# Optimization experiments

Measured on AMD Instinct MI355X. Metric: run time of the kernel, lower is better.

Reference implementation:

```python
import jax, jax.numpy as jnp
import numpy as np

N_NODES = 50000
N_EDGES = 800000
IN_FEATS = 128
H_FEATS = 128
NUM_CLASSES = 64


def _linear_params(key, fan_in, fan_out):
    kw, kb = jax.random.split(key)
    bound = 1.0 / np.sqrt(fan_in)
    W = jax.random.uniform(kw, (fan_out, fan_in), minval=-bound, maxval=bound, dtype=jnp.float32)
    b = jax.random.uniform(kb, (fan_out,), minval=-bound, maxval=bound, dtype=jnp.float32)
    return W, b


def setup_inputs() -> dict:
    key = jax.random.key(0)
    k_feat, k_src, k_dst, k1, k2, k3 = jax.random.split(key, 6)
    in_feat = jax.random.normal(k_feat, (N_NODES, IN_FEATS), dtype=jnp.float32)
    src = jax.random.randint(k_src, (N_EDGES,), 0, N_NODES, dtype=jnp.int32)
    dst = jax.random.randint(k_dst, (N_EDGES,), 0, N_NODES, dtype=jnp.int32)
    W1, b1 = _linear_params(k1, IN_FEATS, H_FEATS)
    W2, b2 = _linear_params(k2, H_FEATS, H_FEATS)
    W3, b3 = _linear_params(k3, H_FEATS, NUM_CLASSES)
    return {"in_feat": in_feat, "W1": W1, "b1": b1, "W2": W2, "b2": b2,
            "W3": W3, "b3": b3, "src": src, "dst": dst}


def reference(in_feat, W1, b1, W2, b2, W3, b3, src, dst):
    N = in_feat.shape[0]

    def gin_layer(x, W, b):
        # DGL GINConv with eps=0: (x + sum of in-neighbor messages) -> Linear
        agg = jax.ops.segment_sum(x[src], dst, num_segments=N)  # [N, d]
        return jax.nn.relu((x + agg) @ W.T + b)

    h = gin_layer(in_feat, W1, b1)
    h = gin_layer(h, W2, b2)
    h = gin_layer(h, W3, b3)
    return h
```

## Files before the change

kernel.cpp:

```cpp
#include <hip/hip_runtime.h>

typedef _Float16 half8 __attribute__((ext_vector_type(8)));
typedef _Float16 half2v __attribute__((ext_vector_type(2)));
typedef float floatx4 __attribute__((ext_vector_type(4)));
typedef unsigned int uintx4 __attribute__((ext_vector_type(4)));

union AB { uint4 u; half8 h; };
union H2 { unsigned int u; _Float16 h[2]; };
union H2P { unsigned int u; half2v h; };

#define CAPLOG 6
#define CAP 64

__global__ __launch_bounds__(256) void histA_init_k(
    const int* __restrict__ dst, int* __restrict__ histG, int E, int nbins,
    const float* __restrict__ W1, const float* __restrict__ W2, const float* __restrict__ W3,
    _Float16* __restrict__ W1h, _Float16* __restrict__ W2h, _Float16* __restrict__ W3h,
    _Float16* __restrict__ z1, _Float16* __restrict__ h1, _Float16* __restrict__ hZ,
    int n4w1, int n4w2, int n4w3, int zoff128, int zoff64) {
    int t = threadIdx.x;
    if (blockIdx.x < 256) {
        __shared__ int h[256];
        h[t] = 0;
        __syncthreads();
        int per = (E + 255) / 256;
        int beg = blockIdx.x * per;
        int end = min(E, beg + per);
        for (int e = beg + t; e < end; e += 256)
            atomicAdd(&h[dst[e] >> 8], 1);
        __syncthreads();
        for (int i = t; i < nbins; i += 256)
            histG[i * 256 + blockIdx.x] = h[i];
        return;
    }
    int i = (blockIdx.x - 256) * 256 + t;
    const float* X;
    _Float16* O;
    int j;
    if (i < n4w1) { X = W1; O = W1h; j = i; }
    else if (i < n4w1 + n4w2) { X = W2; O = W2h; j = i - n4w1; }
    else if (i < n4w1 + n4w2 + n4w3) { X = W3; O = W3h; j = i - n4w1 - n4w2; }
    else {
        int z = i - (n4w1 + n4w2 + n4w3);
        if (z < 16) ((uint4*)z1)[zoff128 + z] = make_uint4(0, 0, 0, 0);
        else if (z < 32) ((uint4*)h1)[zoff128 + (z - 16)] = make_uint4(0, 0, 0, 0);
        else if (z < 40) ((uint4*)hZ)[zoff64 + (z - 32)] = make_uint4(0, 0, 0, 0);
        return;
    }
    float4 v = reinterpret_cast<const float4*>(X)[j];
    union { uint2 u; _Float16 h[4]; } o;
    o.h[0] = (_Float16)v.x; o.h[1] = (_Float16)v.y;
    o.h[2] = (_Float16)v.z; o.h[3] = (_Float16)v.w;
    reinterpret_cast<uint2*>(O)[j] = o.u;
}

__global__ __launch_bounds__(1024) void scan1_k(const int* __restrict__ x,
                                                int* __restrict__ inc,
                                                int* __restrict__ partial, int n) {
    __shared__ int sd[1024];
    int t = threadIdx.x;
    int v = blockIdx.x * 1024 + t;
    sd[t] = (v < n) ? x[v] : 0;
    __syncthreads();
    for (int off = 1; off < 1024; off <<= 1) {
        int val = (t >= off) ? sd[t - off] : 0;
        __syncthreads();
        sd[t] += val;
        __syncthreads();
    }
    if (v < n) inc[v] = sd[t];
    if (t == 1023) partial[blockIdx.x] = sd[1023];
}

__global__ __launch_bounds__(256) void scatgemm_k(
    const int* __restrict__ src, const int* __restrict__ dst,
    const int* __restrict__ inc, const int* __restrict__ histG,
    const int* __restrict__ partial, int nparts,
    unsigned int* __restrict__ binned, int E, int nbins,
    const float* __restrict__ X, const _Float16* __restrict__ Wh,
    _Float16* __restrict__ z1, int nnodes) {
    constexpr int WSTR = 136;
    __shared__ _Float16 Wl[128 * WSTR];

    const int t = threadIdx.x;
    if (blockIdx.x < 256) {
        int* cur = (int*)Wl;
        int* pp = cur + 256;
        int blk = blockIdx.x;
        if (t < 64) {
            int v = (t < nparts) ? partial[t] : 0;
            for (int off = 1; off < 64; off <<= 1) {
                int n = __shfl_up(v, off, 64);
                if (t >= off) v += n;
            }
            int ex = __shfl_up(v, 1, 64);
            if (t == 0) ex = 0;
            pp[t] = ex;
        }
        __syncthreads();
        for (int i = t; i < nbins; i += 256) {
            int idx = i * 256 + blk;
            cur[i] = inc[idx] + pp[idx >> 10] - histG[idx];
        }
        __syncthreads();
        int per = (E + 255) / 256;
        int beg = blk * per;
        int end = min(E, beg + per);
        for (int e = beg + t; e < end; e += 256) {
            int d = dst[e];
            int s = src[e];
            int pos = atomicAdd(&cur[d >> 8], 1);
            binned[pos] = ((unsigned int)(d & 255) << 16) | (unsigned int)s;
        }
        return;
    }

    for (int p = t; p < 128 * 16; p += 256) {
        int f = p >> 4;
        int kq = (p & 15) * 8;
        *reinterpret_cast<uint4*>(&Wl[f * WSTR + kq]) =
            *reinterpret_cast<const uint4*>(Wh + f * 128 + kq);
    }
    __syncthreads();

    const int wave = t >> 6;
    const int lane = t & 63;
    const int quad = lane >> 4;
    const int fcol = lane & 15;
    const int m_base = ((blockIdx.x - 256) * 4 + wave) * 16;
    const int row = m_base + fcol;
    const bool rowok = row < nnodes;

    floatx4 acc[8];
#pragma unroll
    for (int ft = 0; ft < 8; ft++) acc[ft] = (floatx4){0.f, 0.f, 0.f, 0.f};

    const float* Xrow = X + (size_t)row * 128;
#pragma unroll
    for (int step = 0; step < 4; step++) {
        AB a;
        if (rowok) {
            float4 f0 = *reinterpret_cast<const float4*>(Xrow + step * 32 + quad * 8);
            float4 f1 = *reinterpret_cast<const float4*>(Xrow + step * 32 + quad * 8 + 4);
            a.h[0] = (_Float16)f0.x; a.h[1] = (_Float16)f0.y;
            a.h[2] = (_Float16)f0.z; a.h[3] = (_Float16)f0.w;
            a.h[4] = (_Float16)f1.x; a.h[5] = (_Float16)f1.y;
            a.h[6] = (_Float16)f1.z; a.h[7] = (_Float16)f1.w;
        } else a.u = make_uint4(0u, 0u, 0u, 0u);
#pragma unroll
        for (int ft = 0; ft < 8; ft++) {
            half8 b = *reinterpret_cast<const half8*>(
                &Wl[(ft * 16 + fcol) * WSTR + step * 32 + quad * 8]);
            acc[ft] = __builtin_amdgcn_mfma_f32_16x16x32_f16(a.h, b, acc[ft], 0, 0, 0);
        }
    }

#pragma unroll
    for (int ft = 0; ft < 8; ft++) {
        int f = ft * 16 + fcol;
#pragma unroll
        for (int r = 0; r < 4; r++) {
            int node = m_base + quad * 4 + r;
            if (node < nnodes)
                z1[(size_t)node * 128 + f] = (_Float16)acc[ft][r];
        }
    }
}

__global__ __launch_bounds__(256) void binB_k(const unsigned int* __restrict__ binned,
                                              const int* __restrict__ inc,
                                              const int* __restrict__ histG,
                                              const int* __restrict__ partial, int nparts,
                                              unsigned short* __restrict__ col,
                                              int* __restrict__ cnt,
                                              int N, int E, int nbins) {
    __shared__ unsigned short lcol[256 * CAP];
    __shared__ int lcnt[256];
    __shared__ int pp[64];
    __shared__ int bounds[2];
    int t = threadIdx.x;
    int b = blockIdx.x;
    if (t < 64) {
        int v = (t < nparts) ? partial[t] : 0;
        for (int off = 1; off < 64; off <<= 1) {
            int n = __shfl_up(v, off, 64);
            if (t >= off) v += n;
        }
        int ex = __shfl_up(v, 1, 64);
        if (t == 0) ex = 0;
        pp[t] = ex;
    }
    unsigned int* lcol32 = (unsigned int*)lcol;
    for (int i = t; i < 256 * CAP / 2; i += 256) lcol32[i] = 0xFFFFFFFFu;
    lcnt[t] = 0;
    __syncthreads();
    if (t == 0) {
        int i0 = b * 256;
        bounds[0] = inc[i0] + pp[i0 >> 10] - histG[i0];
    } else if (t == 1) {
        if (b == nbins - 1) bounds[1] = E;
        else {
            int i1 = (b + 1) * 256;
            bounds[1] = inc[i1] + pp[i1 >> 10] - histG[i1];
        }
    }
    __syncthreads();
    int beg = bounds[0], end = bounds[1];
    for (int e = beg + t; e < end; e += 256) {
        unsigned int u = binned[e];
        int dl = u >> 16;
        int pos = atomicAdd(&lcnt[dl], 1);
        if (pos < CAP)
            lcol[(dl << CAPLOG) + ((pos & 3) << 4) + (pos >> 2)] = (unsigned short)(u & 0xFFFFu);
    }
    __syncthreads();
    int base = b << 8;
    int nodes = min(256, N - base);
    uint4* colg = (uint4*)(col + ((size_t)base << CAPLOG));
    const uint4* coll = (const uint4*)lcol;
    for (int i = t; i < nodes * 8; i += 256) colg[i] = coll[i];
    for (int i = t; i < nodes; i += 256) cnt[base + i] = lcnt[i];
}

__global__ __launch_bounds__(256) void agg128_k(const _Float16* __restrict__ Z,
                                                const int* __restrict__ cnt,
                                                const unsigned short* __restrict__ col,
                                                const float* __restrict__ bias,
                                                _Float16* __restrict__ H, int nnodes) {
    int w = blockIdx.x * 4 + (threadIdx.x >> 6);
    int lane = threadIdx.x & 63;
    if (w >= nnodes) return;
    const int q = lane >> 4;
    const int c15 = lane & 15;
    const unsigned int* X32 = reinterpret_cast<const unsigned int*>(Z);
    int deg = cnt[w];
    if (deg > CAP) deg = CAP;
    int nb = (deg + 15) >> 4;
    const unsigned short* c = col + ((size_t)w << CAPLOG) + (q << 4);

    H2P a0[4], a1[4], a2[4], a3[4];
#pragma unroll
    for (int m = 0; m < 4; m++) { a0[m].u = 0u; a1[m].u = 0u; a2[m].u = 0u; a3[m].u = 0u; }

    for (int t = 0; t < nb; t++) {
        uint2 iw = *reinterpret_cast<const uint2*>(c + t * 4);
        int s0 = (int)(iw.x & 0xFFFFu); s0 = (s0 < nnodes) ? s0 : nnodes;
        int s1 = (int)(iw.x >> 16);     s1 = (s1 < nnodes) ? s1 : nnodes;
        int s2 = (int)(iw.y & 0xFFFFu); s2 = (s2 < nnodes) ? s2 : nnodes;
        int s3 = (int)(iw.y >> 16);     s3 = (s3 < nnodes) ? s3 : nnodes;
        uint4 v0 = *reinterpret_cast<const uint4*>(X32 + (size_t)s0 * 64 + c15 * 4);
        uint4 v1 = *reinterpret_cast<const uint4*>(X32 + (size_t)s1 * 64 + c15 * 4);
        uint4 v2 = *reinterpret_cast<const uint4*>(X32 + (size_t)s2 * 64 + c15 * 4);
        uint4 v3 = *reinterpret_cast<const uint4*>(X32 + (size_t)s3 * 64 + c15 * 4);
        H2P u;
        u.u = v0.x; a0[0].h += u.h;  u.u = v0.y; a0[1].h += u.h;
        u.u = v0.z; a0[2].h += u.h;  u.u = v0.w; a0[3].h += u.h;
        u.u = v1.x; a1[0].h += u.h;  u.u = v1.y; a1[1].h += u.h;
        u.u = v1.z; a1[2].h += u.h;  u.u = v1.w; a1[3].h += u.h;
        u.u = v2.x; a2[0].h += u.h;  u.u = v2.y; a2[1].h += u.h;
        u.u = v2.z; a2[2].h += u.h;  u.u = v2.w; a2[3].h += u.h;
        u.u = v3.x; a3[0].h += u.h;  u.u = v3.y; a3[1].h += u.h;
        u.u = v3.z; a3[2].h += u.h;  u.u = v3.w; a3[3].h += u.h;
    }
#pragma unroll
    for (int m = 0; m < 4; m++) {
        a0[m].h += a1[m].h;
        a2[m].h += a3[m].h;
        a0[m].h += a2[m].h;
    }
    float fs[8];
#pragma unroll
    for (int m = 0; m < 4; m++) {
        fs[2 * m] = (float)a0[m].h[0];
        fs[2 * m + 1] = (float)a0[m].h[1];
    }
#pragma unroll
    for (int m = 0; m < 8; m++) fs[m] += __shfl_xor(fs[m], 16, 64);
#pragma unroll
    for (int m = 0; m < 8; m++) fs[m] += __shfl_xor(fs[m], 32, 64);

    if (q == 0) {
        uint4 sv = *reinterpret_cast<const uint4*>(X32 + (size_t)w * 64 + c15 * 4);
        H2 x0, x1, x2, x3;
        x0.u = sv.x; x1.u = sv.y; x2.u = sv.z; x3.u = sv.w;
        float o[8];
        o[0] = (float)x0.h[0] + fs[0]; o[1] = (float)x0.h[1] + fs[1];
        o[2] = (float)x1.h[0] + fs[2]; o[3] = (float)x1.h[1] + fs[3];
        o[4] = (float)x2.h[0] + fs[4]; o[5] = (float)x2.h[1] + fs[5];
        o[6] = (float)x3.h[0] + fs[6]; o[7] = (float)x3.h[1] + fs[7];
        if (bias) {
            float4 b0 = *reinterpret_cast<const float4*>(bias + c15 * 8);
            float4 b1 = *reinterpret_cast<const float4*>(bias + c15 * 8 + 4);
            o[0] = fmaxf(o[0] + b0.x, 0.f); o[1] = fmaxf(o[1] + b0.y, 0.f);
            o[2] = fmaxf(o[2] + b0.z, 0.f); o[3] = fmaxf(o[3] + b0.w, 0.f);
            o[4] = fmaxf(o[4] + b1.x, 0.f); o[5] = fmaxf(o[5] + b1.y, 0.f);
            o[6] = fmaxf(o[6] + b1.z, 0.f); o[7] = fmaxf(o[7] + b1.w, 0.f);
        }
        H2 r0, r1, r2, r3;
        r0.h[0] = (_Float16)o[0]; r0.h[1] = (_Float16)o[1];
        r1.h[0] = (_Float16)o[2]; r1.h[1] = (_Float16)o[3];
        r2.h[0] = (_Float16)o[4]; r2.h[1] = (_Float16)o[5];
        r3.h[0] = (_Float16)o[6]; r3.h[1] = (_Float16)o[7];
        uintx4 ov;
        ov.x = r0.u; ov.y = r1.u; ov.z = r2.u; ov.w = r3.u;
        __builtin_nontemporal_store(
            ov, reinterpret_cast<uintx4*>(reinterpret_cast<unsigned int*>(H) +
                                          (size_t)w * 64 + c15 * 4));
    }
}

__global__ __launch_bounds__(256) void agg_final_k(const _Float16* __restrict__ Z,
                                                   const int* __restrict__ cnt,
                                                   const unsigned short* __restrict__ col,
                                                   const float* __restrict__ bias,
                                                   float* __restrict__ out, int nnodes) {
    int lane = threadIdx.x & 63;
    int sub = lane & 31;
    int node = blockIdx.x * 8 + (threadIdx.x >> 6) * 2 + (lane >> 5);
    if (node >= nnodes) return;
    const int q = sub >> 3;
    const int c7 = sub & 7;
    const unsigned int* Z32 = (const unsigned int*)Z;
    int deg = cnt[node];
    if (deg > CAP) deg = CAP;
    int nb = (deg + 15) >> 4;
    const unsigned short* c = col + ((size_t)node << CAPLOG) + (q << 4);

    H2P a0[4], a1[4], a2[4], a3[4];
#pragma unroll
    for (int m = 0; m < 4; m++) { a0[m].u = 0u; a1[m].u = 0u; a2[m].u = 0u; a3[m].u = 0u; }

    for (int t = 0; t < nb; t++) {
        uint2 iw = *reinterpret_cast<const uint2*>(c + t * 4);
        int s0 = (int)(iw.x & 0xFFFFu); s0 = (s0 < nnodes) ? s0 : nnodes;
        int s1 = (int)(iw.x >> 16);     s1 = (s1 < nnodes) ? s1 : nnodes;
        int s2 = (int)(iw.y & 0xFFFFu); s2 = (s2 < nnodes) ? s2 : nnodes;
        int s3 = (int)(iw.y >> 16);     s3 = (s3 < nnodes) ? s3 : nnodes;
        uint4 v0 = *reinterpret_cast<const uint4*>(Z32 + (size_t)s0 * 32 + c7 * 4);
        uint4 v1 = *reinterpret_cast<const uint4*>(Z32 + (size_t)s1 * 32 + c7 * 4);
        uint4 v2 = *reinterpret_cast<const uint4*>(Z32 + (size_t)s2 * 32 + c7 * 4);
        uint4 v3 = *reinterpret_cast<const uint4*>(Z32 + (size_t)s3 * 32 + c7 * 4);
        H2P u;
        u.u = v0.x; a0[0].h += u.h;  u.u = v0.y; a0[1].h += u.h;
        u.u = v0.z; a0[2].h += u.h;  u.u = v0.w; a0[3].h += u.h;
        u.u = v1.x; a1[0].h += u.h;  u.u = v1.y; a1[1].h += u.h;
        u.u = v1.z; a1[2].h += u.h;  u.u = v1.w; a1[3].h += u.h;
        u.u = v2.x; a2[0].h += u.h;  u.u = v2.y; a2[1].h += u.h;
        u.u = v2.z; a2[2].h += u.h;  u.u = v2.w; a2[3].h += u.h;
        u.u = v3.x; a3[0].h += u.h;  u.u = v3.y; a3[1].h += u.h;
        u.u = v3.z; a3[2].h += u.h;  u.u = v3.w; a3[3].h += u.h;
    }
#pragma unroll
    for (int m = 0; m < 4; m++) {
        a0[m].h += a1[m].h;
        a2[m].h += a3[m].h;
        a0[m].h += a2[m].h;
    }
    float fs[8];
#pragma unroll
    for (int m = 0; m < 4; m++) {
        fs[2 * m] = (float)a0[m].h[0];
        fs[2 * m + 1] = (float)a0[m].h[1];
    }
#pragma unroll
    for (int m = 0; m < 8; m++) fs[m] += __shfl_xor(fs[m], 8, 64);
#pragma unroll
    for (int m = 0; m < 8; m++) fs[m] += __shfl_xor(fs[m], 16, 64);

    if (q == 0) {
        uint4 sv = *reinterpret_cast<const uint4*>(Z32 + (size_t)node * 32 + c7 * 4);
        H2 x0, x1, x2, x3;
        x0.u = sv.x; x1.u = sv.y; x2.u = sv.z; x3.u = sv.w;
        float4 b0 = *reinterpret_cast<const float4*>(bias + c7 * 8);
        float4 b1 = *reinterpret_cast<const float4*>(bias + c7 * 8 + 4);
        float4 w0, w1;
        w0.x = fmaxf((float)x0.h[0] + fs[0] + b0.x, 0.f);
        w0.y = fmaxf((float)x0.h[1] + fs[1] + b0.y, 0.f);
        w0.z = fmaxf((float)x1.h[0] + fs[2] + b0.z, 0.f);
        w0.w = fmaxf((float)x1.h[1] + fs[3] + b0.w, 0.f);
        w1.x = fmaxf((float)x2.h[0] + fs[4] + b1.x, 0.f);
        w1.y = fmaxf((float)x2.h[1] + fs[5] + b1.y, 0.f);
        w1.z = fmaxf((float)x3.h[0] + fs[6] + b1.z, 0.f);
        w1.w = fmaxf((float)x3.h[1] + fs[7] + b1.w, 0.f);
        *reinterpret_cast<float4*>(out + (size_t)node * 64 + c7 * 8) = w0;
        *reinterpret_cast<float4*>(out + (size_t)node * 64 + c7 * 8 + 4) = w1;
    }
}

__global__ __launch_bounds__(256) void gemm23_k(const _Float16* __restrict__ Y,
                                                const _Float16* __restrict__ W2h,
                                                const float* __restrict__ b2,
                                                const _Float16* __restrict__ W3h,
                                                _Float16* __restrict__ hZ, int nnodes) {
    constexpr int WSTR = 136;
    __shared__ _Float16 Wl[128 * WSTR];
    __shared__ _Float16 Hl[64 * WSTR];
    __shared__ float Bl[128];

    const int t = threadIdx.x;
    for (int p = t; p < 128 * 16; p += 256) {
        int f = p >> 4;
        int kq = (p & 15) * 8;
        *reinterpret_cast<uint4*>(&Wl[f * WSTR + kq]) =
            *reinterpret_cast<const uint4*>(W2h + f * 128 + kq);
    }
    if (t < 128) Bl[t] = b2[t];
    __syncthreads();

    const int wave = t >> 6;
    const int lane = t & 63;
    const int quad = lane >> 4;
    const int fcol = lane & 15;
    const int m_base = (blockIdx.x * 4 + wave) * 16;
    const int row = m_base + fcol;
    const bool rowok = row < nnodes;

    floatx4 acc[8];
#pragma unroll
    for (int ft = 0; ft < 8; ft++) acc[ft] = (floatx4){0.f, 0.f, 0.f, 0.f};

    const uint4* Yrow = reinterpret_cast<const uint4*>(Y + (size_t)row * 128);
#pragma unroll
    for (int step = 0; step < 4; step++) {
        AB a;
        if (rowok) a.u = Yrow[step * 4 + quad];
        else       a.u = make_uint4(0u, 0u, 0u, 0u);
#pragma unroll
        for (int ft = 0; ft < 8; ft++) {
            half8 b = *reinterpret_cast<const half8*>(
                &Wl[(ft * 16 + fcol) * WSTR + step * 32 + quad * 8]);
            acc[ft] = __builtin_amdgcn_mfma_f32_16x16x32_f16(a.h, b, acc[ft], 0, 0, 0);
        }
    }

#pragma unroll
    for (int ft = 0; ft < 8; ft++) {
        int f = ft * 16 + fcol;
        float bv = Bl[f];
#pragma unroll
        for (int r = 0; r < 4; r++) {
            int nl = wave * 16 + quad * 4 + r;
            Hl[nl * WSTR + f] = (_Float16)fmaxf(acc[ft][r] + bv, 0.f);
        }
    }
    __syncthreads();

    for (int p = t; p < 64 * 16; p += 256) {
        int f = p >> 4;
        int kq = (p & 15) * 8;
        *reinterpret_cast<uint4*>(&Wl[f * WSTR + kq]) =
            *reinterpret_cast<const uint4*>(W3h + f * 128 + kq);
    }
    __syncthreads();

    floatx4 acc2[4];
#pragma unroll
    for (int ft = 0; ft < 4; ft++) acc2[ft] = (floatx4){0.f, 0.f, 0.f, 0.f};
#pragma unroll
    for (int step = 0; step < 4; step++) {
        AB a;
        a.h = *reinterpret_cast<const half8*>(
            &Hl[(wave * 16 + fcol) * WSTR + step * 32 + quad * 8]);
#pragma unroll
        for (int ft = 0; ft < 4; ft++) {
            half8 b = *reinterpret_cast<const half8*>(
                &Wl[(ft * 16 + fcol) * WSTR + step * 32 + quad * 8]);
            acc2[ft] = __builtin_amdgcn_mfma_f32_16x16x32_f16(a.h, b, acc2[ft], 0, 0, 0);
        }
    }
#pragma unroll
    for (int ft = 0; ft < 4; ft++) {
        int f = ft * 16 + fcol;
#pragma unroll
        for (int r = 0; r < 4; r++) {
            int node = m_base + quad * 4 + r;
            if (node < nnodes)
                hZ[(size_t)node * 64 + f] = (_Float16)acc2[ft][r];
        }
    }
}

extern "C" void kernel_launch(void* const* d_in, const int* in_sizes, int n_in,
                              void* d_out, int out_size, void* d_ws, size_t ws_size,
                              hipStream_t stream) {
    const float* in_feat = (const float*)d_in[0];
    const float* W1 = (const float*)d_in[1];
    const float* b1 = (const float*)d_in[2];
    const float* W2 = (const float*)d_in[3];
    const float* b2 = (const float*)d_in[4];
    const float* W3 = (const float*)d_in[5];
    const float* b3 = (const float*)d_in[6];
    const int* src = (const int*)d_in[7];
    const int* dst = (const int*)d_in[8];
    float* out = (float*)d_out;

    const int N = in_sizes[0] / 128;
    const int E = in_sizes[7];
    const int szW1 = in_sizes[1];
    const int szW2 = in_sizes[3];
    const int szW3 = in_sizes[5];
    const int nbins = (N + 255) >> 8;
    const int nhist = nbins * 256;

    char* p = (char*)d_ws;
    int* cnt = (int*)p;               p += (size_t)N * 4;
    unsigned short* col = (unsigned short*)p; p += (size_t)N * CAP * 2;
    int* histG = (int*)p;             p += (size_t)nhist * 4;
    int* incS = (int*)p;              p += (size_t)nhist * 4;
    int* partial = (int*)p;           p += 256;
    unsigned int* binned = (unsigned int*)p; p += (size_t)E * 4;
    _Float16* z1 = (_Float16*)p;      p += (size_t)(N + 1) * 128 * 2;
    _Float16* h1 = (_Float16*)p;      p += (size_t)(N + 1) * 128 * 2;
    _Float16* hB = (_Float16*)p;      p += (size_t)N * 128 * 2;
    _Float16* hZ = (_Float16*)p;      p += (size_t)(N + 1) * 64 * 2;
    _Float16* W1h = (_Float16*)p;     p += (size_t)szW1 * 2;
    _Float16* W2h = (_Float16*)p;     p += (size_t)szW2 * 2;
    _Float16* W3h = (_Float16*)p;     p += (size_t)szW3 * 2;

    const int nblk_scan = (nhist + 1023) / 1024;
    const int nblk_gemm = (N + 63) / 64;
    const int nblk_agg = (N + 3) / 4;

    {
        int total = szW1 / 4 + szW2 / 4 + szW3 / 4 + 40;
        int iblk = (total + 255) / 256;
        histA_init_k<<<256 + iblk, 256, 0, stream>>>(dst, histG, E, nbins,
                                                     W1, W2, W3, W1h, W2h, W3h,
                                                     z1, h1, hZ,
                                                     szW1 / 4, szW2 / 4, szW3 / 4,
                                                     N * 16, N * 8);
    }
    scan1_k<<<nblk_scan, 1024, 0, stream>>>(histG, incS, partial, nhist);
    scatgemm_k<<<256 + nblk_gemm, 256, 0, stream>>>(src, dst, incS, histG, partial,
                                                    nblk_scan, binned, E, nbins,
                                                    in_feat, W1h, z1, N);
    binB_k<<<nbins, 256, 0, stream>>>(binned, incS, histG, partial, nblk_scan,
                                      col, cnt, N, E, nbins);
    agg128_k<<<nblk_agg, 256, 0, stream>>>(z1, cnt, col, b1, h1, N);
    agg128_k<<<nblk_agg, 256, 0, stream>>>(h1, cnt, col, nullptr, hB, N);
    gemm23_k<<<nblk_gemm, 256, 0, stream>>>(hB, W2h, b2, W3h, hZ, N);
    agg_final_k<<<(N + 7) / 8, 256, 0, stream>>>(hZ, cnt, col, b3, out, N);
}
```

Baseline: 223.9 us.

## Split aggregation feature dimension across two blocks and widen neighbor parallelism per wave

The aggregation kernels now split each node's feature row into two halves handled by separate blocks, doubling the grid. Within a wave, more lane groups each process fewer neighbors: 8 groups of 2 neighbors for agg128 and 16 groups of 1 for the final layer. To keep index loads contiguous per group, the CSR column layout is re-interleaved with stride 8 instead of 4. This raises memory-level parallelism and occupancy at the cost of an extra shuffle reduction stage and duplicated index and count loads per half.

After: 269.6 us. 20.4% more time.

```diff
diff --git a/kernel.cpp b/kernel.cpp
--- a/kernel.cpp
+++ b/kernel.cpp
@@ -211,7 +211,7 @@
         int dl = u >> 16;
         int pos = atomicAdd(&lcnt[dl], 1);
         if (pos < CAP)
-            lcol[(dl << CAPLOG) + ((pos & 3) << 4) + (pos >> 2)] = (unsigned short)(u & 0xFFFFu);
+            lcol[(dl << CAPLOG) + ((pos & 7) << 3) + (pos >> 3)] = (unsigned short)(u & 0xFFFFu);
     }
     __syncthreads();
     int base = b << 8;
@@ -227,47 +227,38 @@
                                                 const unsigned short* __restrict__ col,
                                                 const float* __restrict__ bias,
                                                 _Float16* __restrict__ H, int nnodes) {
-    int w = blockIdx.x * 4 + (threadIdx.x >> 6);
+    const int half = blockIdx.x & 1;
+    int w = (blockIdx.x >> 1) * 4 + (threadIdx.x >> 6);
     int lane = threadIdx.x & 63;
     if (w >= nnodes) return;
-    const int q = lane >> 4;
-    const int c15 = lane & 15;
+    const int o = lane >> 3;
+    const int c7 = lane & 7;
     const unsigned int* X32 = reinterpret_cast<const unsigned int*>(Z);
     int deg = cnt[w];
     if (deg > CAP) deg = CAP;
     int nb = (deg + 15) >> 4;
-    const unsigned short* c = col + ((size_t)w << CAPLOG) + (q << 4);
-
-    H2P a0[4], a1[4], a2[4], a3[4];
-#pragma unroll
-    for (int m = 0; m < 4; m++) { a0[m].u = 0u; a1[m].u = 0u; a2[m].u = 0u; a3[m].u = 0u; }
+    const unsigned short* c = col + ((size_t)w << CAPLOG) + (o << 3);
+    const int xoff = half * 32 + c7 * 4;
+
+    H2P a0[4], a1[4];
+#pragma unroll
+    for (int m = 0; m < 4; m++) { a0[m].u = 0u; a1[m].u = 0u; }
 
     for (int t = 0; t < nb; t++) {
-        uint2 iw = *reinterpret_cast<const uint2*>(c + t * 4);
-        int s0 = (int)(iw.x & 0xFFFFu); s0 = (s0 < nnodes) ? s0 : nnodes;
-        int s1 = (int)(iw.x >> 16);     s1 = (s1 < nnodes) ? s1 : nnodes;
-        int s2 = (int)(iw.y & 0xFFFFu); s2 = (s2 < nnodes) ? s2 : nnodes;
-        int s3 = (int)(iw.y >> 16);     s3 = (s3 < nnodes) ? s3 : nnodes;
-        uint4 v0 = *reinterpret_cast<const uint4*>(X32 + (size_t)s0 * 64 + c15 * 4);
-        uint4 v1 = *reinterpret_cast<const uint4*>(X32 + (size_t)s1 * 64 + c15 * 4);
-        uint4 v2 = *reinterpret_cast<const uint4*>(X32 + (size_t)s2 * 64 + c15 * 4);
-        uint4 v3 = *reinterpret_cast<const uint4*>(X32 + (size_t)s3 * 64 + c15 * 4);
+        unsigned int iw = *reinterpret_cast<const unsigned int*>(c + 2 * t);
+        int s0 = (int)(iw & 0xFFFFu); s0 = (s0 < nnodes) ? s0 : nnodes;
+        int s1 = (int)(iw >> 16);     s1 = (s1 < nnodes) ? s1 : nnodes;
+        uint4 v0 = *reinterpret_cast<const uint4*>(X32 + (size_t)s0 * 64 + xoff);
+        uint4 v1 = *reinterpret_cast<const uint4*>(X32 + (size_t)s1 * 64 + xoff);
         H2P u;
         u.u = v0.x; a0[0].h += u.h;  u.u = v0.y; a0[1].h += u.h;
         u.u = v0.z; a0[2].h += u.h;  u.u = v0.w; a0[3].h += u.h;
         u.u = v1.x; a1[0].h += u.h;  u.u = v1.y; a1[1].h += u.h;
         u.u = v1.z; a1[2].h += u.h;  u.u = v1.w; a1[3].h += u.h;
-        u.u = v2.x; a2[0].h += u.h;  u.u = v2.y; a2[1].h += u.h;
-        u.u = v2.z; a2[2].h += u.h;  u.u = v2.w; a2[3].h += u.h;
-        u.u = v3.x; a3[0].h += u.h;  u.u = v3.y; a3[1].h += u.h;
-        u.u = v3.z; a3[2].h += u.h;  u.u = v3.w; a3[3].h += u.h;
-    }
-#pragma unroll
-    for (int m = 0; m < 4; m++) {
-        a0[m].h += a1[m].h;
-        a2[m].h += a3[m].h;
-        a0[m].h += a2[m].h;
-    }
+    }
+#pragma unroll
+    for (int m = 0; m < 4; m++) a0[m].h += a1[m].h;
+
     float fs[8];
 #pragma unroll
     for (int m = 0; m < 4; m++) {
@@ -275,37 +266,39 @@
         fs[2 * m + 1] = (float)a0[m].h[1];
     }
 #pragma unroll
+    for (int m = 0; m < 8; m++) fs[m] += __shfl_xor(fs[m], 8, 64);
+#pragma unroll
     for (int m = 0; m < 8; m++) fs[m] += __shfl_xor(fs[m], 16, 64);
 #pragma unroll
     for (int m = 0; m < 8; m++) fs[m] += __shfl_xor(fs[m], 32, 64);
 
-    if (q == 0) {
-        uint4 sv = *reinterpret_cast<const uint4*>(X32 + (size_t)w * 64 + c15 * 4);
+    if (o == 0) {
+        uint4 sv = *reinterpret_cast<const uint4*>(X32 + (size_t)w * 64 + xoff);
         H2 x0, x1, x2, x3;
         x0.u = sv.x; x1.u = sv.y; x2.u = sv.z; x3.u = sv.w;
-        float o[8];
-        o[0] = (float)x0.h[0] + fs[0]; o[1] = (float)x0.h[1] + fs[1];
-        o[2] = (float)x1.h[0] + fs[2]; o[3] = (float)x1.h[1] + fs[3];
-        o[4] = (float)x2.h[0] + fs[4]; o[5] = (float)x2.h[1] + fs[5];
-        o[6] = (float)x3.h[0] + fs[6]; o[7] = (float)x3.h[1] + fs[7];
+        float out8[8];
+        out8[0] = (float)x0.h[0] + fs[0]; out8[1] = (float)x0.h[1] + fs[1];
+        out8[2] = (float)x1.h[0] + fs[2]; out8[3] = (float)x1.h[1] + fs[3];
+        out8[4] = (float)x2.h[0] + fs[4]; out8[5] = (float)x2.h[1] + fs[5];
+        out8[6] = (float)x3.h[0] + fs[6]; out8[7] = (float)x3.h[1] + fs[7];
         if (bias) {
-            float4 b0 = *reinterpret_cast<const float4*>(bias + c15 * 8);
-            float4 b1 = *reinterpret_cast<const float4*>(bias + c15 * 8 + 4);
-            o[0] = fmaxf(o[0] + b0.x, 0.f); o[1] = fmaxf(o[1] + b0.y, 0.f);
-            o[2] = fmaxf(o[2] + b0.z, 0.f); o[3] = fmaxf(o[3] + b0.w, 0.f);
-            o[4] = fmaxf(o[4] + b1.x, 0.f); o[5] = fmaxf(o[5] + b1.y, 0.f);
-            o[6] = fmaxf(o[6] + b1.z, 0.f); o[7] = fmaxf(o[7] + b1.w, 0.f);
+            float4 b0 = *reinterpret_cast<const float4*>(bias + half * 64 + c7 * 8);
+            float4 b1 = *reinterpret_cast<const float4*>(bias + half * 64 + c7 * 8 + 4);
+            out8[0] = fmaxf(out8[0] + b0.x, 0.f); out8[1] = fmaxf(out8[1] + b0.y, 0.f);
+            out8[2] = fmaxf(out8[2] + b0.z, 0.f); out8[3] = fmaxf(out8[3] + b0.w, 0.f);
+            out8[4] = fmaxf(out8[4] + b1.x, 0.f); out8[5] = fmaxf(out8[5] + b1.y, 0.f);
+            out8[6] = fmaxf(out8[6] + b1.z, 0.f); out8[7] = fmaxf(out8[7] + b1.w, 0.f);
         }
         H2 r0, r1, r2, r3;
-        r0.h[0] = (_Float16)o[0]; r0.h[1] = (_Float16)o[1];
-        r1.h[0] = (_Float16)o[2]; r1.h[1] = (_Float16)o[3];
-        r2.h[0] = (_Float16)o[4]; r2.h[1] = (_Float16)o[5];
-        r3.h[0] = (_Float16)o[6]; r3.h[1] = (_Float16)o[7];
+        r0.h[0] = (_Float16)out8[0]; r0.h[1] = (_Float16)out8[1];
+        r1.h[0] = (_Float16)out8[2]; r1.h[1] = (_Float16)out8[3];
+        r2.h[0] = (_Float16)out8[4]; r2.h[1] = (_Float16)out8[5];
+        r3.h[0] = (_Float16)out8[6]; r3.h[1] = (_Float16)out8[7];
         uintx4 ov;
         ov.x = r0.u; ov.y = r1.u; ov.z = r2.u; ov.w = r3.u;
         __builtin_nontemporal_store(
             ov, reinterpret_cast<uintx4*>(reinterpret_cast<unsigned int*>(H) +
-                                          (size_t)w * 64 + c15 * 4));
+                                          (size_t)w * 64 + xoff));
     }
 }
 
@@ -314,65 +307,52 @@
                                                    const unsigned short* __restrict__ col,
                                                    const float* __restrict__ bias,
                                                    float* __restrict__ out, int nnodes) {
+    const int half = blockIdx.x & 1;
+    int w = (blockIdx.x >> 1) * 4 + (threadIdx.x >> 6);
     int lane = threadIdx.x & 63;
-    int sub = lane & 31;
-    int node = blockIdx.x * 8 + (threadIdx.x >> 6) * 2 + (lane >> 5);
-    if (node >= nnodes) return;
-    const int q = sub >> 3;
-    const int c7 = sub & 7;
+    if (w >= nnodes) return;
+    const int g = lane >> 2;
+    const int c3 = lane & 3;
     const unsigned int* Z32 = (const unsigned int*)Z;
-    int deg = cnt[node];
+    int deg = cnt[w];
     if (deg > CAP) deg = CAP;
     int nb = (deg + 15) >> 4;
-    const unsigned short* c = col + ((size_t)node << CAPLOG) + (q << 4);
-
-    H2P a0[4], a1[4], a2[4], a3[4];
-#pragma unroll
-    for (int m = 0; m < 4; m++) { a0[m].u = 0u; a1[m].u = 0u; a2[m].u = 0u; a3[m].u = 0u; }
+    const unsigned short* c = col + ((size_t)w << CAPLOG) + ((g & 7) << 3) + (g >> 3);
+    const int xoff = half * 16 + c3 * 4;
+
+    H2P a[4];
+#pragma unroll
+    for (int m = 0; m < 4; m++) a[m].u = 0u;
 
     for (int t = 0; t < nb; t++) {
-        uint2 iw = *reinterpret_cast<const uint2*>(c + t * 4);
-        int s0 = (int)(iw.x & 0xFFFFu); s0 = (s0 < nnodes) ? s0 : nnodes;
-        int s1 = (int)(iw.x >> 16);     s1 = (s1 < nnodes) ? s1 : nnodes;
-        int s2 = (int)(iw.y & 0xFFFFu); s2 = (s2 < nnodes) ? s2 : nnodes;
-        int s3 = (int)(iw.y >> 16);     s3 = (s3 < nnodes) ? s3 : nnodes;
-        uint4 v0 = *reinterpret_cast<const uint4*>(Z32 + (size_t)s0 * 32 + c7 * 4);
-        uint4 v1 = *reinterpret_cast<const uint4*>(Z32 + (size_t)s1 * 32 + c7 * 4);
-        uint4 v2 = *reinterpret_cast<const uint4*>(Z32 + (size_t)s2 * 32 + c7 * 4);
-        uint4 v3 = *reinterpret_cast<const uint4*>(Z32 + (size_t)s3 * 32 + c7 * 4);
+        int s = (int)c[2 * t];
+        s = (s < nnodes) ? s : nnodes;
+        uint4 v = *reinterpret_cast<const uint4*>(Z32 + (size_t)s * 32 + xoff);
         H2P u;
-        u.u = v0.x; a0[0].h += u.h;  u.u = v0.y; a0[1].h += u.h;
-        u.u = v0.z; a0[2].h += u.h;  u.u = v0.w; a0[3].h += u.h;
-        u.u = v1.x; a1[0].h += u.h;  u.u = v1.y; a1[1].h += u.h;
-        u.u = v1.z; a1[2].h += u.h;  u.u = v1.w; a1[3].h += u.h;
-        u.u = v2.x; a2[0].h += u.h;  u.u = v2.y; a2[1].h += u.h;
-        u.u = v2.z; a2[2].h += u.h;  u.u = v2.w; a2[3].h += u.h;
-        u.u = v3.x; a3[0].h += u.h;  u.u = v3.y; a3[1].h += u.h;
-        u.u = v3.z; a3[2].h += u.h;  u.u = v3.w; a3[3].h += u.h;
-    }
+        u.u = v.x; a[0].h += u.h;  u.u = v.y; a[1].h += u.h;
+        u.u = v.z; a[2].h += u.h;  u.u = v.w; a[3].h += u.h;
+    }
+    float fs[8];
 #pragma unroll
     for (int m = 0; m < 4; m++) {
-        a0[m].h += a1[m].h;
-        a2[m].h += a3[m].h;
-        a0[m].h += a2[m].h;
-    }
-    float fs[8];
-#pragma unroll
-    for (int m = 0; m < 4; m++) {
-        fs[2 * m] = (float)a0[m].h[0];
-        fs[2 * m + 1] = (float)a0[m].h[1];
-    }
+        fs[2 * m] = (float)a[m].h[0];
+        fs[2 * m + 1] = (float)a[m].h[1];
+    }
+#pragma unroll
+    for (int m = 0; m < 8; m++) fs[m] += __shfl_xor(fs[m], 4, 64);
 #pragma unroll
     for (int m = 0; m < 8; m++) fs[m] += __shfl_xor(fs[m], 8, 64);
 #pragma unroll
     for (int m = 0; m < 8; m++) fs[m] += __shfl_xor(fs[m], 16, 64);
-
-    if (q == 0) {
-        uint4 sv = *reinterpret_cast<const uint4*>(Z32 + (size_t)node * 32 + c7 * 4);
+#pragma unroll
+    for (int m = 0; m < 8; m++) fs[m] += __shfl_xor(fs[m], 32, 64);
+
+    if (g == 0) {
+        uint4 sv = *reinterpret_cast<const uint4*>(Z32 + (size_t)w * 32 + xoff);
         H2 x0, x1, x2, x3;
         x0.u = sv.x; x1.u = sv.y; x2.u = sv.z; x3.u = sv.w;
-        float4 b0 = *reinterpret_cast<const float4*>(bias + c7 * 8);
-        float4 b1 = *reinterpret_cast<const float4*>(bias + c7 * 8 + 4);
+        float4 b0 = *reinterpret_cast<const float4*>(bias + half * 32 + c3 * 8);
+        float4 b1 = *reinterpret_cast<const float4*>(bias + half * 32 + c3 * 8 + 4);
         float4 w0, w1;
         w0.x = fmaxf((float)x0.h[0] + fs[0] + b0.x, 0.f);
         w0.y = fmaxf((float)x0.h[1] + fs[1] + b0.y, 0.f);
@@ -382,8 +362,8 @@
         w1.y = fmaxf((float)x2.h[1] + fs[5] + b1.y, 0.f);
         w1.z = fmaxf((float)x3.h[0] + fs[6] + b1.z, 0.f);
         w1.w = fmaxf((float)x3.h[1] + fs[7] + b1.w, 0.f);
-        *reinterpret_cast<float4*>(out + (size_t)node * 64 + c7 * 8) = w0;
-        *reinterpret_cast<float4*>(out + (size_t)node * 64 + c7 * 8 + 4) = w1;
+        *reinterpret_cast<float4*>(out + (size_t)w * 64 + half * 32 + c3 * 8) = w0;
+        *reinterpret_cast<float4*>(out + (size_t)w * 64 + half * 32 + c3 * 8 + 4) = w1;
     }
 }
 
@@ -519,7 +499,7 @@
 
     const int nblk_scan = (nhist + 1023) / 1024;
     const int nblk_gemm = (N + 63) / 64;
-    const int nblk_agg = (N + 3) / 4;
+    const int nblk_agg = ((N + 3) / 4) * 2;
 
     {
         int total = szW1 / 4 + szW2 / 4 + szW3 / 4 + 40;
@@ -539,5 +519,5 @@
     agg128_k<<<nblk_agg, 256, 0, stream>>>(z1, cnt, col, b1, h1, N);
     agg128_k<<<nblk_agg, 256, 0, stream>>>(h1, cnt, col, nullptr, hB, N);
     gemm23_k<<<nblk_gemm, 256, 0, stream>>>(hB, W2h, b2, W3h, hZ, N);
-    agg_final_k<<<(N + 7) / 8, 256, 0, stream>>>(hZ, cnt, col, b3, out, N);
-}
+    agg_final_k<<<nblk_agg, 256, 0, stream>>>(hZ, cnt, col, b3, out, N);
+}
```
